# Kernel optimization log

Measured on AMD Instinct MI355X. Metric: run time of the kernel, lower is better.

## Reference

```python
import jax, jax.numpy as jnp
import numpy as np

T = 1_500_000   # traindata rows
N = 2_000_000   # neighbor rows
n = 1_048_576   # layer's n (divisible by 4)
m = 1           # layer's m (sort column)
NEG_INIT = -100000.0


def setup_inputs() -> dict:
    key = jax.random.key(0)
    k1, k2, k3, k4, k5 = jax.random.split(key, 5)
    feats = jax.random.normal(k1, (T, 3), dtype=jnp.float32)
    # col 0: node ID = arange(T); cols 1:4: features
    traindata = jnp.concatenate([jnp.arange(T, dtype=jnp.float32)[:, None], feats], axis=1)
    ids = jax.random.randint(k2, (N,), 0, T).astype(jnp.float32)      # col 0: IDs into traindata
    sortcol = jax.random.normal(k3, (N,), dtype=jnp.float32)          # col m=1: sort key
    mid = jax.random.normal(k4, (N, 2), dtype=jnp.float32)            # cols 2,3
    flag = jax.random.randint(k5, (N,), 0, 10).astype(jnp.float32)
    neighbor = jnp.stack([ids, sortcol, mid[:, 0], mid[:, 1], flag], axis=1)
    return {"traindata": traindata, "neighbor": neighbor}


def reference(traindata, neighbor):
    # tf.nn.top_k(bt, k=full, sorted=True) == stable descending sort
    bt = neighbor[:, m]
    order = jnp.argsort(-bt)          # stable -> ties keep original index order, like top_k
    data = neighbor[order]
    new_neighbor = data[neighbor.shape[0] - n:]   # bottom-n rows [n, 5]

    # rows of new_neighbor whose flag (col 4) == 0: append their IDs, gathered from the
    # ORIGINAL neighbor col 0 (as in the source), padded with 3 zero feature cols.
    zero_mask = new_neighbor[:, 4] == 0
    idx = jnp.nonzero(zero_mask, size=n, fill_value=0)[0]        # static-size for jit
    valid = jnp.arange(n) < jnp.sum(zero_mask)
    rev_ids = jnp.where(valid, neighbor[idx, 0], jnp.float32(-1.0))  # -1 never matches a real ID
    rev = jnp.concatenate([rev_ids[:, None], jnp.zeros((n, 3), neighbor.dtype)], axis=1)
    td = jnp.concatenate([traindata, rev], axis=0)               # [T+n, 4]
    tdlist = td[:, 0]

    # tp[e] = FIRST index where tdlist == new_neighbor[e, 0]
    # stable argsort + searchsorted(left) gives the smallest original index among equals
    sort_idx = jnp.argsort(tdlist)
    sv = tdlist[sort_idx]
    pos = jnp.searchsorted(sv, new_neighbor[:, 0], side='left')
    tp = sort_idx[pos]                                           # [n]

    max_ = jnp.max(td[tp, 1:], axis=1)                           # [n] row-wise feature max
    flags = new_neighbor[:, 4]

    G = n // 4
    tp_g = tp.reshape(G, 4)
    max_g = max_.reshape(G, 4)
    flag_g = flags.reshape(G, 4)

    # sequential 4-step recurrence per group (mirrors the j-loop with tf.cond):
    # update iff (flag != 0) == (max_ > maxmin)
    maxmin = jnp.full((G,), NEG_INIT, dtype=max_.dtype)
    maxindex = jnp.full((G,), -100, dtype=tp.dtype)
    for j in range(4):
        re1 = flag_g[:, j] != 0
        gt = max_g[:, j] > maxmin
        re = re1 == gt
        maxmin = jnp.where(re, max_g[:, j], maxmin)
        maxindex = jnp.where(re, tp_g[:, j], maxindex)

    # gather surviving traindata rows (clip guards the never-updated -100 sentinel,
    # which would be an error in the original TF graph)
    out = td[jnp.clip(maxindex, 0, td.shape[0] - 1)]             # [G, 4]
    return out
```

## Files before the change

kernel.cpp:

```cpp
#include <hip/hip_runtime.h>
#include <stdint.h>

#define T_ROWS 1500000
#define N_ROWS 2000000
#define N_SEL  1048576
#define G_CNT  (N_SEL/4)
#define LB     (N_ROWS - N_SEL)
#define TILE   8192
#define NBLK   ((N_ROWS + TILE - 1)/TILE)
#define NBLK1  (NBLK + 1)
#define STHREADS 1024
#define SWAVES 16
#define WTILE  (TILE/SWAVES)
#define WROUNDS (WTILE/64)
#define HTHREADS 512
#define BINS   256
#define NB_MX  ((T_ROWS + HTHREADS - 1)/HTHREADS)

static_assert((uint64_t)NBLK * TILE >= N_ROWS, "tile coverage");
static_assert(TILE % (SWAVES * 64) == 0, "wave partition");
static_assert(NBLK <= 256, "one block per CU (balance)");
static_assert(T_ROWS < (1 << 21), "tp fits 21 bits");
static_assert((LB * 4) % 16 == 0, "finalize uint4 alignment");

__global__ __launch_bounds__(HTHREADS) void build_all(
        const float* __restrict__ nb, const float* __restrict__ td,
        uint64_t* __restrict__ codes, float* __restrict__ mxtab,
        uint32_t* __restrict__ gH) {
    const int b = blockIdx.x;
    if (b >= NBLK) {
        int i = (b - NBLK) * HTHREADS + threadIdx.x;
        if (i < T_ROWS) {
            float4 r = *(const float4*)(td + (size_t)i * 4);
            mxtab[i] = fmaxf(r.y, fmaxf(r.z, r.w));
        }
        return;
    }
    __shared__ uint32_t h[BINS];
    const int t = threadIdx.x;
    if (t < BINS) h[t] = 0;
    __syncthreads();
    const int base = b * TILE;
    #pragma unroll
    for (int r = 0; r < TILE / HTHREADS; ++r) {
        int i = base + r * HTHREADS + t;
        if (i < N_ROWS) {
            const float* row = nb + (size_t)i * 5;
            uint32_t u = __float_as_uint(row[1]);
            uint32_t ku = (u & 0x80000000u) ? ~u : (u | 0x80000000u);
            uint32_t kd = ~ku;
            uint32_t tp = (uint32_t)(int)row[0];
            uint32_t fl = (row[4] != 0.0f) ? 1u : 0u;
            codes[i] = ((uint64_t)kd << 32) | (fl << 21) | tp;
            atomicAdd(&h[kd & (BINS - 1)], 1u);
        }
    }
    __syncthreads();
    if (t < BINS) gH[(size_t)t * NBLK1 + b] = h[t];
}

template <int SHIFT32>
__global__ __launch_bounds__(HTHREADS) void radix_hist_u(
        const uint64_t* __restrict__ src, uint32_t* __restrict__ gH) {
    __shared__ uint32_t h[BINS];
    const int t = threadIdx.x;
    if (t < BINS) h[t] = 0;
    __syncthreads();
    const uint4* s4 = (const uint4*)(src + (size_t)blockIdx.x * TILE);
    const int pairBase = blockIdx.x * (TILE / 2);
    #pragma unroll
    for (int r = 0; r < TILE / (2 * HTHREADS); ++r) {
        int j = r * HTHREADS + t;
        uint4 v = s4[j];
        int i0 = (pairBase + j) * 2;
        if (i0 < N_ROWS)     atomicAdd(&h[(v.y >> SHIFT32) & (BINS - 1)], 1u);
        if (i0 + 1 < N_ROWS) atomicAdd(&h[(v.w >> SHIFT32) & (BINS - 1)], 1u);
    }
    __syncthreads();
    if (t < BINS) gH[(size_t)t * NBLK1 + blockIdx.x] = h[t];
}

template <int SHIFT32>
__global__ __launch_bounds__(HTHREADS) void radix_hist_s(
        const uint64_t* __restrict__ src, uint32_t* __restrict__ gH) {
    __shared__ uint32_t h[BINS];
    const int t = threadIdx.x;
    const int lane = t & 63;
    if (t < BINS) h[t] = 0;
    __syncthreads();
    const int base = blockIdx.x * TILE;
    const uint32_t* s32 = (const uint32_t*)src;
    #pragma unroll
    for (int r = 0; r < TILE / HTHREADS; ++r) {
        int i = base + r * HTHREADS + t;
        bool active = (i < N_ROWS);
        uint32_t d = 0;
        if (active) d = (s32[2 * (size_t)i + 1] >> SHIFT32) & (BINS - 1);
        uint64_t m = __ballot(active ? 1 : 0);
        #pragma unroll
        for (int bb = 0; bb < 8; ++bb) {
            uint64_t x = __ballot((active && ((d >> bb) & 1u)) ? 1 : 0);
            m = ((d >> bb) & 1u) ? (m & x) : (m & ~x);
        }
        int ldr = __ffsll((unsigned long long)m) - 1;
        if (active && lane == ldr) atomicAdd(&h[d], (uint32_t)__popcll(m));
    }
    __syncthreads();
    if (t < BINS) gH[(size_t)t * NBLK1 + blockIdx.x] = h[t];
}

__global__ void radix_rowscan(uint32_t* __restrict__ gH) {
    const int d = blockIdx.x;
    const int lane = threadIdx.x;
    uint32_t* row = gH + (size_t)d * NBLK1;
    uint32_t carry = 0;
    for (int b0 = 0; b0 < NBLK; b0 += 64) {
        int i = b0 + lane;
        uint32_t v = (i < NBLK) ? row[i] : 0u;
        uint32_t s = v;
        #pragma unroll
        for (int off = 1; off < 64; off <<= 1) {
            uint32_t tt = __shfl_up(s, off, 64);
            if (lane >= off) s += tt;
        }
        if (i < NBLK) row[i] = s - v + carry;
        carry += __shfl(s, 63, 64);
    }
    if (lane == 0) row[NBLK] = carry;
}

template <int SHIFT, bool LAST>
__global__ __launch_bounds__(STHREADS) void radix_scatter(
        const uint64_t* __restrict__ src, uint64_t* __restrict__ dst,
        uint32_t* __restrict__ dst32, const uint32_t* __restrict__ gH) {
    __shared__ uint64_t tileS[TILE];
    __shared__ uint32_t cnt32[SWAVES * BINS];
    __shared__ uint32_t writeBase[BINS];
    __shared__ uint32_t wpT[SWAVES], wpL[SWAVES];

    const int t = threadIdx.x;
    const int lane = t & 63;
    const int w = t >> 6;
    const int blk = blockIdx.x;
    const int base = blk * TILE;
    const int tileCount = (N_ROWS - base < TILE) ? (N_ROWS - base) : TILE;

    uint32_t rp = 0, lc = 0, tot = 0;
    if (t < BINS) {
        const uint32_t* row = gH + (size_t)t * NBLK1;
        rp = row[blk];
        lc = row[blk + 1] - rp;
        tot = row[NBLK];
    }

    #pragma unroll
    for (int k = t; k < SWAVES * BINS; k += STHREADS) cnt32[k] = 0u;
    __syncthreads();

    uint64_t creg[WROUNDS];
    uint32_t meta[WROUNDS];
    const uint64_t below = (lane == 0) ? 0ull : (~0ull >> (64 - lane));
    #pragma unroll
    for (int r = 0; r < WROUNDS; ++r) {
        int idx = base + w * WTILE + r * 64 + lane;
        bool active = (idx < N_ROWS);
        uint64_t c = active ? src[idx] : 0ull;
        creg[r] = c;
        uint32_t d = (uint32_t)(c >> SHIFT) & (BINS - 1);
        uint64_t m = __ballot(active ? 1 : 0);
        #pragma unroll
        for (int bb = 0; bb < 8; ++bb) {
            uint64_t x = __ballot((active && ((d >> bb) & 1u)) ? 1 : 0);
            m = ((d >> bb) & 1u) ? (m & x) : (m & ~x);
        }
        int ldr = __ffsll((unsigned long long)m) - 1;
        uint32_t cnt = (uint32_t)__popcll(m);
        uint32_t rank = (uint32_t)__popcll(m & below);
        meta[r] = rank | ((uint32_t)(ldr < 0 ? 0 : ldr) << 8) | (cnt << 16);
        if (active && lane == ldr)
            atomicAdd(&cnt32[w * BINS + d], cnt);
    }
    __syncthreads();

    uint32_t sT = tot, sL = lc;
    #pragma unroll
    for (int off = 1; off < 64; off <<= 1) {
        uint32_t aT = __shfl_up(sT, off, 64);
        uint32_t aL = __shfl_up(sL, off, 64);
        if (lane >= off) { sT += aT; sL += aL; }
    }
    if (lane == 63) { wpT[w] = sT; wpL[w] = sL; }
    __syncthreads();
    uint32_t exT = sT - tot, exL = sL - lc;
    #pragma unroll
    for (int wv = 0; wv < SWAVES; ++wv) if (wv < w) { exT += wpT[wv]; exL += wpL[wv]; }

    if (t < BINS) {
        writeBase[t] = exT + rp - exL;
        uint32_t run = exL;
        #pragma unroll
        for (int wv = 0; wv < SWAVES; ++wv) {
            uint32_t c0 = cnt32[wv * BINS + t];
            cnt32[wv * BINS + t] = run;
            run += c0;
        }
    }
    __syncthreads();

    #pragma unroll
    for (int r = 0; r < WROUNDS; ++r) {
        int idx = base + w * WTILE + r * 64 + lane;
        bool active = (idx < N_ROWS);
        uint64_t c = creg[r];
        uint32_t d = (uint32_t)(c >> SHIFT) & (BINS - 1);
        uint32_t mt = meta[r];
        uint32_t rank = mt & 0xFFu;
        int ldr = (int)((mt >> 8) & 0xFFu);
        uint32_t cnt = mt >> 16;
        uint32_t before = 0;
        if (active && lane == ldr)
            before = atomicAdd(&cnt32[w * BINS + d], cnt);
        before = __shfl(before, ldr, 64);
        if (active) tileS[before + rank] = c;
    }
    __syncthreads();

    #pragma unroll
    for (int r = 0; r < TILE / STHREADS; ++r) {
        int p = r * STHREADS + t;
        if (p < tileCount) {
            uint64_t c = tileS[p];
            uint32_t d = (uint32_t)(c >> SHIFT) & (BINS - 1);
            uint32_t g = writeBase[d] + p;
            if (!LAST) {
                dst[(size_t)g] = c;
            } else if (g >= LB) {
                dst32[g] = (uint32_t)c;
            }
        }
    }
}

__global__ void finalize(const uint32_t* __restrict__ pay, const float* __restrict__ td,
                         const float* __restrict__ mxtab, float* __restrict__ out) {
    int g = blockIdx.x * 256 + threadIdx.x;
    if (g >= G_CNT) return;
    uint4 p4 = *(const uint4*)(pay + LB + (size_t)g * 4);
    uint32_t cs[4] = {p4.x, p4.y, p4.z, p4.w};
    float maxmin = -100000.0f;
    int maxindex = -100;
    #pragma unroll
    for (int j = 0; j < 4; ++j) {
        int tp = (int)(cs[j] & 0x1FFFFFu);
        bool re1 = ((cs[j] >> 21) & 1u) != 0u;
        float mx = mxtab[tp];
        bool gt = (mx > maxmin);
        if (re1 == gt) { maxmin = mx; maxindex = tp; }
    }
    int mi = maxindex < 0 ? 0 : maxindex;
    float4 row = *(const float4*)(td + (size_t)mi * 4);
    *(float4*)(out + (size_t)g * 4) = row;
}

extern "C" void kernel_launch(void* const* d_in, const int* in_sizes, int n_in,
                              void* d_out, int out_size, void* d_ws, size_t ws_size,
                              hipStream_t stream) {
    const float* td = (const float*)d_in[0];
    const float* nb = (const float*)d_in[1];
    float* out = (float*)d_out;
    uint8_t* ws = (uint8_t*)d_ws;

    float*    mxtab = (float*)(ws);
    uint32_t* gH    = (uint32_t*)(ws + (size_t)6 * 1024 * 1024);
    uint64_t* A     = (uint64_t*)(ws + (size_t)8 * 1024 * 1024);
    uint64_t* B     = (uint64_t*)(ws + (size_t)24 * 1024 * 1024);

    build_all<<<NBLK + NB_MX, HTHREADS, 0, stream>>>(nb, td, A, mxtab, gH);

    radix_rowscan<<<BINS, 64, 0, stream>>>(gH);
    radix_scatter<32, false><<<NBLK, STHREADS, 0, stream>>>(A, B, nullptr, gH);

    radix_hist_u<8><<<NBLK, HTHREADS, 0, stream>>>(B, gH);
    radix_rowscan<<<BINS, 64, 0, stream>>>(gH);
    radix_scatter<40, false><<<NBLK, STHREADS, 0, stream>>>(B, A, nullptr, gH);

    radix_hist_u<16><<<NBLK, HTHREADS, 0, stream>>>(A, gH);
    radix_rowscan<<<BINS, 64, 0, stream>>>(gH);
    radix_scatter<48, false><<<NBLK, STHREADS, 0, stream>>>(A, B, nullptr, gH);

    radix_hist_s<24><<<NBLK, HTHREADS, 0, stream>>>(B, gH);
    radix_rowscan<<<BINS, 64, 0, stream>>>(gH);
    radix_scatter<56, true><<<NBLK, STHREADS, 0, stream>>>(B, nullptr, (uint32_t*)A, gH);

    finalize<<<(G_CNT + 255) / 256, 256, 0, stream>>>((const uint32_t*)A, td, mxtab, out);
}
```

Baseline: 129.6 us.

## Fuse radix row-scan into histogram kernels via atomic-counter spin wait

Removes the four separate radix_rowscan launches by appending 256 extra blocks to each histogram kernel. These blocks spin on a per-pass atomic counter until all histogram blocks have published, then scan one digit row each. A tiny zero_cnts kernel resets the counters at the start of each run. This saves three kernel launches and their gaps, but the spin wait only stays deadlock-free if the histogram blocks get scheduled alongside the waiting scan blocks.

```diff
diff --git a/kernel.cpp b/kernel.cpp
--- a/kernel.cpp
+++ b/kernel.cpp
@@ -22,12 +22,50 @@
 static_assert(NBLK <= 256, "one block per CU (balance)");
 static_assert(T_ROWS < (1 << 21), "tp fits 21 bits");
 static_assert((LB * 4) % 16 == 0, "finalize uint4 alignment");
+static_assert(NBLK + 256 <= 1024, "hist+scan co-residency (spin safety)");
+
+__global__ void zero_cnts(uint32_t* __restrict__ cnts) {
+    cnts[threadIdx.x * 64] = 0u;
+}
+
+__device__ __forceinline__ void scan_block(uint32_t* __restrict__ gH,
+                                           uint32_t* __restrict__ cnt, int digit) {
+    const int t = threadIdx.x;
+    if (t == 0) {
+        while (__hip_atomic_load(cnt, __ATOMIC_RELAXED, __HIP_MEMORY_SCOPE_AGENT) < NBLK)
+            __builtin_amdgcn_s_sleep(1);
+        (void)__hip_atomic_load(cnt, __ATOMIC_ACQUIRE, __HIP_MEMORY_SCOPE_AGENT);
+    }
+    __syncthreads();
+    if (t < 64) {
+        const int lane = t;
+        uint32_t* row = gH + (size_t)digit * NBLK1;
+        uint32_t carry = 0;
+        for (int b0 = 0; b0 < NBLK; b0 += 64) {
+            int i = b0 + lane;
+            uint32_t v = (i < NBLK) ? row[i] : 0u;
+            uint32_t s = v;
+            #pragma unroll
+            for (int off = 1; off < 64; off <<= 1) {
+                uint32_t tt = __shfl_up(s, off, 64);
+                if (lane >= off) s += tt;
+            }
+            if (i < NBLK) row[i] = s - v + carry;
+            carry += __shfl(s, 63, 64);
+        }
+        if (lane == 0) row[NBLK] = carry;
+    }
+}
 
 __global__ __launch_bounds__(HTHREADS) void build_all(
         const float* __restrict__ nb, const float* __restrict__ td,
         uint64_t* __restrict__ codes, float* __restrict__ mxtab,
-        uint32_t* __restrict__ gH) {
+        uint32_t* __restrict__ gH, uint32_t* __restrict__ cnts) {
     const int b = blockIdx.x;
+    if (b >= NBLK + NB_MX) {
+        scan_block(gH, &cnts[0], b - (NBLK + NB_MX));
+        return;
+    }
     if (b >= NBLK) {
         int i = (b - NBLK) * HTHREADS + threadIdx.x;
         if (i < T_ROWS) {
@@ -57,17 +95,23 @@
     }
     __syncthreads();
     if (t < BINS) gH[(size_t)t * NBLK1 + b] = h[t];
-}
-
-template <int SHIFT32>
+    __syncthreads();
+    if (t == 0)
+        __hip_atomic_fetch_add(&cnts[0], 1u, __ATOMIC_RELEASE, __HIP_MEMORY_SCOPE_AGENT);
+}
+
+template <int SHIFT32, int PASS>
 __global__ __launch_bounds__(HTHREADS) void radix_hist_u(
-        const uint64_t* __restrict__ src, uint32_t* __restrict__ gH) {
+        const uint64_t* __restrict__ src, uint32_t* __restrict__ gH,
+        uint32_t* __restrict__ cnts) {
+    const int b = blockIdx.x;
+    if (b >= NBLK) { scan_block(gH, &cnts[PASS * 64], b - NBLK); return; }
     __shared__ uint32_t h[BINS];
     const int t = threadIdx.x;
     if (t < BINS) h[t] = 0;
     __syncthreads();
-    const uint4* s4 = (const uint4*)(src + (size_t)blockIdx.x * TILE);
-    const int pairBase = blockIdx.x * (TILE / 2);
+    const uint4* s4 = (const uint4*)(src + (size_t)b * TILE);
+    const int pairBase = b * (TILE / 2);
     #pragma unroll
     for (int r = 0; r < TILE / (2 * HTHREADS); ++r) {
         int j = r * HTHREADS + t;
@@ -77,18 +121,24 @@
         if (i0 + 1 < N_ROWS) atomicAdd(&h[(v.w >> SHIFT32) & (BINS - 1)], 1u);
     }
     __syncthreads();
-    if (t < BINS) gH[(size_t)t * NBLK1 + blockIdx.x] = h[t];
-}
-
-template <int SHIFT32>
+    if (t < BINS) gH[(size_t)t * NBLK1 + b] = h[t];
+    __syncthreads();
+    if (t == 0)
+        __hip_atomic_fetch_add(&cnts[PASS * 64], 1u, __ATOMIC_RELEASE, __HIP_MEMORY_SCOPE_AGENT);
+}
+
+template <int SHIFT32, int PASS>
 __global__ __launch_bounds__(HTHREADS) void radix_hist_s(
-        const uint64_t* __restrict__ src, uint32_t* __restrict__ gH) {
+        const uint64_t* __restrict__ src, uint32_t* __restrict__ gH,
+        uint32_t* __restrict__ cnts) {
+    const int b = blockIdx.x;
+    if (b >= NBLK) { scan_block(gH, &cnts[PASS * 64], b - NBLK); return; }
     __shared__ uint32_t h[BINS];
     const int t = threadIdx.x;
     const int lane = t & 63;
     if (t < BINS) h[t] = 0;
     __syncthreads();
-    const int base = blockIdx.x * TILE;
+    const int base = b * TILE;
     const uint32_t* s32 = (const uint32_t*)src;
     #pragma unroll
     for (int r = 0; r < TILE / HTHREADS; ++r) {
@@ -106,27 +156,10 @@
         if (active && lane == ldr) atomicAdd(&h[d], (uint32_t)__popcll(m));
     }
     __syncthreads();
-    if (t < BINS) gH[(size_t)t * NBLK1 + blockIdx.x] = h[t];
-}
-
-__global__ void radix_rowscan(uint32_t* __restrict__ gH) {
-    const int d = blockIdx.x;
-    const int lane = threadIdx.x;
-    uint32_t* row = gH + (size_t)d * NBLK1;
-    uint32_t carry = 0;
-    for (int b0 = 0; b0 < NBLK; b0 += 64) {
-        int i = b0 + lane;
-        uint32_t v = (i < NBLK) ? row[i] : 0u;
-        uint32_t s = v;
-        #pragma unroll
-        for (int off = 1; off < 64; off <<= 1) {
-            uint32_t tt = __shfl_up(s, off, 64);
-            if (lane >= off) s += tt;
-        }
-        if (i < NBLK) row[i] = s - v + carry;
-        carry += __shfl(s, 63, 64);
-    }
-    if (lane == 0) row[NBLK] = carry;
+    if (t < BINS) gH[(size_t)t * NBLK1 + b] = h[t];
+    __syncthreads();
+    if (t == 0)
+        __hip_atomic_fetch_add(&cnts[PASS * 64], 1u, __ATOMIC_RELEASE, __HIP_MEMORY_SCOPE_AGENT);
 }
 
 template <int SHIFT, bool LAST>
@@ -272,24 +305,22 @@
 
     float*    mxtab = (float*)(ws);
     uint32_t* gH    = (uint32_t*)(ws + (size_t)6 * 1024 * 1024);
+    uint32_t* cnts  = (uint32_t*)(ws + (size_t)6 * 1024 * 1024 + 384 * 1024);
     uint64_t* A     = (uint64_t*)(ws + (size_t)8 * 1024 * 1024);
     uint64_t* B     = (uint64_t*)(ws + (size_t)24 * 1024 * 1024);
 
-    build_all<<<NBLK + NB_MX, HTHREADS, 0, stream>>>(nb, td, A, mxtab, gH);
-
-    radix_rowscan<<<BINS, 64, 0, stream>>>(gH);
+    zero_cnts<<<1, 64, 0, stream>>>(cnts);
+
+    build_all<<<NBLK + NB_MX + 256, HTHREADS, 0, stream>>>(nb, td, A, mxtab, gH, cnts);
     radix_scatter<32, false><<<NBLK, STHREADS, 0, stream>>>(A, B, nullptr, gH);
 
-    radix_hist_u<8><<<NBLK, HTHREADS, 0, stream>>>(B, gH);
-    radix_rowscan<<<BINS, 64, 0, stream>>>(gH);
+    radix_hist_u<8, 1><<<NBLK + 256, HTHREADS, 0, stream>>>(B, gH, cnts);
     radix_scatter<40, false><<<NBLK, STHREADS, 0, stream>>>(B, A, nullptr, gH);
 
-    radix_hist_u<16><<<NBLK, HTHREADS, 0, stream>>>(A, gH);
-    radix_rowscan<<<BINS, 64, 0, stream>>>(gH);
+    radix_hist_u<16, 2><<<NBLK + 256, HTHREADS, 0, stream>>>(A, gH, cnts);
     radix_scatter<48, false><<<NBLK, STHREADS, 0, stream>>>(A, B, nullptr, gH);
 
-    radix_hist_s<24><<<NBLK, HTHREADS, 0, stream>>>(B, gH);
-    radix_rowscan<<<BINS, 64, 0, stream>>>(gH);
+    radix_hist_s<24, 3><<<NBLK + 256, HTHREADS, 0, stream>>>(B, gH, cnts);
     radix_scatter<56, true><<<NBLK, STHREADS, 0, stream>>>(B, nullptr, (uint32_t*)A, gH);
 
     finalize<<<(G_CNT + 255) / 256, 256, 0, stream>>>((const uint32_t*)A, td, mxtab, out);
```

After: 222.1 us. 71.5% more time.
